# Kernel optimization log

Measured on AMD Instinct MI355X. Metric: run time of the kernel, lower is better.

Reference implementation:

```python
import math
import jax, jax.numpy as jnp
import numpy as np

B, S, E, H = 1, 2048, 2048, 16
HD = E // H // 2            # qk head dim = 64
DEPTH = 12
LAMBDA_INIT = 0.8 - 0.6 * math.exp(-0.3 * DEPTH)
EPS = 1e-5
NEG = -1e30

# rotary table (non-learned buffer), interleaved pairs, dim = HD
_pos = np.arange(S, dtype=np.float32)[:, None]
_div = np.exp(np.arange(0, HD, 2, dtype=np.float32) * (-math.log(10000.0) / HD))
COS = jnp.asarray(np.cos(_pos * _div))  # [S, HD/2]
SIN = jnp.asarray(np.sin(_pos * _div))


def _rope_interleaved(x):
    # x: [B, S, nH, HD]; rotate interleaved pairs (x0,x1),(x2,x3),...
    x1 = x[..., 0::2]
    x2 = x[..., 1::2]
    c = COS[None, :, None, :]
    s = SIN[None, :, None, :]
    o1 = x1 * c - x2 * s
    o2 = x1 * s + x2 * c
    return jnp.stack([o1, o2], axis=-1).reshape(x.shape)


def _causal_attn(q, k, v):
    # q,k: [B,S,H,Dk]; v: [B,S,H,Dv]; flash_attn default scale = Dk**-0.5
    scale = q.shape[-1] ** -0.5
    scores = jnp.einsum('bqhd,bkhd->bhqk', q, k) * scale
    mask = jnp.tril(jnp.ones((S, S), dtype=bool))
    scores = jnp.where(mask[None, None], scores, NEG)
    p = jax.nn.softmax(scores, axis=-1)
    return jnp.einsum('bhqk,bkhd->bqhd', p, v)


def setup_inputs() -> dict:
    key = jax.random.key(0)
    ks = jax.random.split(key, 10)
    w = lambda k: jax.random.normal(k, (E, E), dtype=jnp.float32) * 0.02
    lam = lambda k: jax.random.normal(k, (HD,), dtype=jnp.float32) * 0.1
    return {
        'x': jax.random.normal(ks[0], (B, S, E), dtype=jnp.float32),
        'Wq': w(ks[1]), 'Wk': w(ks[2]), 'Wv': w(ks[3]), 'Wo': w(ks[4]),
        'lq1': lam(ks[5]), 'lk1': lam(ks[6]), 'lq2': lam(ks[7]), 'lk2': lam(ks[8]),
        'g': jnp.ones((2 * HD,), dtype=jnp.float32),  # RMSNorm affine weight
    }


def reference(x, Wq, Wk, Wv, Wo, lq1, lk1, lq2, lk2, g):
    q = (x @ Wq).reshape(B, S, 2 * H, HD)
    k = (x @ Wk).reshape(B, S, 2 * H, HD)
    v = (x @ Wv).reshape(B, S, H, 2 * HD)
    q = _rope_interleaved(q).reshape(B, S, H, 2, HD)
    k = _rope_interleaved(k).reshape(B, S, H, 2, HD)
    q1, q2 = q[:, :, :, 0], q[:, :, :, 1]
    k1, k2 = k[:, :, :, 0], k[:, :, :, 1]
    attn1 = _causal_attn(q1, k1, v)  # [B,S,H,2*HD]
    attn2 = _causal_attn(q2, k2, v)
    lambda_full = (jnp.exp(jnp.sum(lq1 * lk1)) - jnp.exp(jnp.sum(lq2 * lk2))
                   + LAMBDA_INIT)
    a = attn1 - lambda_full * attn2
    # RMSNorm over last dim (2*HD) with affine weight g
    a = a * jax.lax.rsqrt(jnp.mean(a * a, axis=-1, keepdims=True) + EPS) * g
    a = a * (1.0 - LAMBDA_INIT)
    a = a.reshape(B, S, E)
    return a @ Wo
```

## Files before the change

kernel.cpp:

```cpp
#include <hip/hip_runtime.h>

typedef unsigned short u16;
typedef __bf16 bf16x8 __attribute__((ext_vector_type(8)));
typedef float f32x4 __attribute__((ext_vector_type(4)));

#define LAMBDA_INIT_F 0.7836057665f
#define ONE_MINUS_LI  0.2163942335f
#define Q_PRESCALE 0.1803368801f

__device__ __forceinline__ u16 f2bf(float f) {
  union { float f; unsigned u; } v; v.f = f;
  unsigned r = v.u + 0x7fffu + ((v.u >> 16) & 1u);
  return (u16)(r >> 16);
}

__device__ __forceinline__ float fast_exp2(float x) {
#if __has_builtin(__builtin_amdgcn_exp2f)
  return __builtin_amdgcn_exp2f(x);
#else
  return __builtin_exp2f(x);
#endif
}

__device__ __forceinline__ void gload_lds16(const void* g, void* l) {
  __builtin_amdgcn_global_load_lds(
      (const __attribute__((address_space(1))) void*)g,
      (__attribute__((address_space(3))) void*)l, 16, 0, 0);
}

__global__ __launch_bounds__(256) void cast_x_kernel(const float* __restrict__ x,
                                                     u16* __restrict__ xb) {
  const int i = (blockIdx.x * 256 + threadIdx.x) * 4;
  const float4 v = *(const float4*)(x + i);
  u16 tmp[4] = {f2bf(v.x), f2bf(v.y), f2bf(v.z), f2bf(v.w)};
  *(uint2*)(xb + i) = *(const uint2*)tmp;
}

__global__ __launch_bounds__(256) void transpose_w_kernel(
    const float* __restrict__ Wq, const float* __restrict__ Wk,
    const float* __restrict__ Wv, const float* __restrict__ Wo,
    u16* __restrict__ WqkvT, u16* __restrict__ WoT) {
  __shared__ float t[32][33];
  const int z = blockIdx.z;
  const float* src = (z == 0) ? Wq : (z == 1) ? Wk : (z == 2) ? Wv : Wo;
  const int n0 = blockIdx.x * 32, k0 = blockIdx.y * 32;
  const int tx = threadIdx.x & 31, ty = threadIdx.x >> 5;
#pragma unroll
  for (int i = 0; i < 4; ++i)
    t[ty + i * 8][tx] = src[(size_t)(k0 + ty + i * 8) * 2048 + n0 + tx];
  __syncthreads();
  u16* dst = (z < 3) ? (WqkvT + ((size_t)z * 2048 + n0) * 2048 + k0)
                     : (WoT + (size_t)n0 * 2048 + k0);
#pragma unroll
  for (int i = 0; i < 4; ++i)
    dst[(size_t)(ty + i * 8) * 2048 + tx] = f2bf(t[tx][ty + i * 8]);
}

__global__ __launch_bounds__(256) void rope_table_kernel(float* __restrict__ cosT,
                                                         float* __restrict__ sinT) {
  const int idx = blockIdx.x * 256 + threadIdx.x;
  const int s = idx >> 5, i = idx & 31;
  const float div = expf((float)(2 * i) * (-9.210340371976184f / 64.f));
  const float ang = (float)s * div;
  cosT[idx] = cosf(ang);
  sinT[idx] = sinf(ang);
}

__global__ void lambda_kernel(const float* __restrict__ lq1, const float* __restrict__ lk1,
                              const float* __restrict__ lq2, const float* __restrict__ lk2,
                              float* __restrict__ lam) {
  const int t = threadIdx.x;
  float p1 = lq1[t] * lk1[t];
  float p2 = lq2[t] * lk2[t];
#pragma unroll
  for (int mk = 1; mk < 64; mk <<= 1) {
    p1 += __shfl_xor(p1, mk);
    p2 += __shfl_xor(p2, mk);
  }
  if (t == 0) *lam = expf(p1) - expf(p2) + LAMBDA_INIT_F;
}

__global__ __launch_bounds__(256) void gemm_bt_kernel(
    const u16* __restrict__ A, const u16* __restrict__ Bt,
    float* __restrict__ C, int M, int N, int K) {
  __shared__ u16 As[2][128 * 64];
  __shared__ u16 Bs[2][128 * 64];
  const int tid = threadIdx.x;
  const int lane = tid & 63;
  const int w = tid >> 6;
  const int wm = w >> 1, wn = w & 1;
  const long m0 = (long)blockIdx.y * 128;
  const long n0 = (long)blockIdx.x * 128;

  f32x4 acc[4][4];
#pragma unroll
  for (int i = 0; i < 4; ++i)
#pragma unroll
    for (int j = 0; j < 4; ++j) acc[i][j] = f32x4{0.f, 0.f, 0.f, 0.f};

  const int sr = lane >> 3;
  const int scS = ((lane & 7) ^ sr) * 8;
  const int fr = lane & 15;
  const int kgrp = lane >> 4;
  const int swz = (fr & 7) << 3;

  const u16* aSrc = A + (m0 + w * 32 + sr) * (long)K + scS;
  const u16* bSrc = Bt + (n0 + w * 32 + sr) * (long)K + scS;

  auto stage = [&](int b, long koff) {
#pragma unroll
    for (int g = 0; g < 4; ++g) {
      gload_lds16(aSrc + koff + (size_t)g * 8 * K, &As[b][(w * 32 + g * 8) * 64]);
      gload_lds16(bSrc + koff + (size_t)g * 8 * K, &Bs[b][(w * 32 + g * 8) * 64]);
    }
  };

  stage(0, 0);
  __syncthreads();
  int cur = 0;
  for (int k0 = 0; k0 < K; k0 += 64) {
    if (k0 + 64 < K) stage(cur ^ 1, k0 + 64);
    __builtin_amdgcn_s_setprio(1);
#pragma unroll
    for (int ks = 0; ks < 2; ++ks) {
      bf16x8 af[4], bfr[4];
#pragma unroll
      for (int mi = 0; mi < 4; ++mi)
        af[mi] = *(const bf16x8*)&As[cur][(wm * 64 + mi * 16 + fr) * 64 +
                                          ((ks * 32 + kgrp * 8) ^ swz)];
#pragma unroll
      for (int ni = 0; ni < 4; ++ni)
        bfr[ni] = *(const bf16x8*)&Bs[cur][(wn * 64 + ni * 16 + fr) * 64 +
                                           ((ks * 32 + kgrp * 8) ^ swz)];
#pragma unroll
      for (int mi = 0; mi < 4; ++mi)
#pragma unroll
        for (int ni = 0; ni < 4; ++ni)
          acc[mi][ni] =
              __builtin_amdgcn_mfma_f32_16x16x32_bf16(af[mi], bfr[ni], acc[mi][ni], 0, 0, 0);
    }
    __builtin_amdgcn_s_setprio(0);
    __syncthreads();
    cur ^= 1;
  }
  const int rg = (lane >> 4) * 4;
#pragma unroll
  for (int mi = 0; mi < 4; ++mi)
#pragma unroll
    for (int ni = 0; ni < 4; ++ni) {
      const long col = n0 + wn * 64 + ni * 16 + fr;
#pragma unroll
      for (int j = 0; j < 4; ++j) {
        const long row = m0 + wm * 64 + mi * 16 + rg + j;
        C[row * N + col] = acc[mi][ni][j];
      }
    }
}

__global__ __launch_bounds__(256) void rope_apply_kernel(
    const float* __restrict__ proj, const float* __restrict__ cosT,
    const float* __restrict__ sinT, u16* __restrict__ Qh, u16* __restrict__ Kh) {
  const int s = blockIdx.x;
  const int tid = threadIdx.x;
#pragma unroll
  for (int t = 0; t < 8; ++t) {
    const int p = t * 256 + tid;
    const int isK = p >> 10;
    const int pp = p & 1023;
    const int hh = pp >> 5, i = pp & 31;
    const float* src = proj + (size_t)s * 6144 + isK * 2048 + hh * 64 + 2 * i;
    const float x1 = src[0], x2 = src[1];
    const float c = cosT[s * 32 + i], sn = sinT[s * 32 + i];
    const float scl = isK ? 1.0f : Q_PRESCALE;
    u16* dst = (isK ? Kh : Qh) + ((size_t)hh * 2048 + s) * 64 + 2 * i;
    dst[0] = f2bf((x1 * c - x2 * sn) * scl);
    dst[1] = f2bf((x1 * sn + x2 * c) * scl);
  }
}

__global__ __launch_bounds__(256) void transpose_v_kernel(const float* __restrict__ proj,
                                                          u16* __restrict__ Vt) {
  __shared__ float t[32][33];
  const int s0 = blockIdx.x * 32, r0 = blockIdx.y * 32;
  const int tx = threadIdx.x & 31, ty = threadIdx.x >> 5;
#pragma unroll
  for (int i = 0; i < 4; ++i)
    t[ty + i * 8][tx] = proj[(size_t)(s0 + ty + i * 8) * 6144 + 4096 + r0 + tx];
  __syncthreads();
#pragma unroll
  for (int i = 0; i < 4; ++i)
    Vt[(size_t)(r0 + ty + i * 8) * 2048 + s0 + tx] = f2bf(t[tx][ty + i * 8]);
}

__global__ __launch_bounds__(256) void attn_kernel(
    const u16* __restrict__ Qh, const u16* __restrict__ Kh,
    const u16* __restrict__ Vt, float* __restrict__ attnOut) {
  __shared__ u16 Kt[2][64 * 64];
  __shared__ u16 Vs[2][128 * 64];
  __shared__ __bf16 Ps[4 * 16 * 64];
  const int tid = threadIdx.x, lane = tid & 63, w = tid >> 6;
  const int fr = lane & 15, kgrp = lane >> 4;
  const int bid = blockIdx.x;
  const int xcd = bid & 7, idx = bid >> 3;
  const int hh = xcd * 4 + (idx & 3);
  const int pairIdx = idx >> 2;
  const int h = hh >> 1, comp = hh & 1;
  const int q0A = pairIdx * 64, q0B = (31 - pairIdx) * 64;
  const int jmaxA = pairIdx, jmaxB = 31 - pairIdx;
  const int ntA = jmaxA + 1, ntot = ntA + jmaxB + 1;

  const int sr = lane >> 3;
  const int scS = (((lane & 7) ^ sr) * 8);
  const int swz = (fr & 7) << 3;

  bf16x8 qf0, qf1;
  {
    const u16* qb = Qh + ((size_t)hh * 2048 + q0A + w * 16 + fr) * 64 + kgrp * 8;
    qf0 = *(const bf16x8*)qb;
    qf1 = *(const bf16x8*)(qb + 32);
  }
  bf16x8 onesf;
#pragma unroll
  for (int i = 0; i < 8; ++i) onesf[i] = (__bf16)1.0f;

  f32x4 o[9];
#pragma unroll
  for (int i = 0; i < 9; ++i) o[i] = f32x4{0.f, 0.f, 0.f, 0.f};
  float m_r[4] = {-1e30f, -1e30f, -1e30f, -1e30f};

  auto stage = [&](int b, int kv0) {
#pragma unroll
    for (int i = 0; i < 2; ++i)
      gload_lds16(Kh + ((size_t)hh * 2048 + kv0 + i * 32 + w * 8 + sr) * 64 + scS,
                  &Kt[b][(i * 32 + w * 8) * 64]);
#pragma unroll
    for (int i = 0; i < 4; ++i)
      gload_lds16(Vt + ((size_t)h * 128 + i * 32 + w * 8 + sr) * 2048 + kv0 + scS,
                  &Vs[b][(i * 32 + w * 8) * 64]);
  };

  auto writeOut = [&](int q0) {
    float* outp = attnOut + (size_t)comp * (2048 * 2048);
#pragma unroll
    for (int j = 0; j < 4; ++j) {
      const int row = q0 + w * 16 + kgrp * 4 + j;
      const float inv = 1.0f / o[8][j];
      float* op = outp + (size_t)row * 2048 + h * 128;
#pragma unroll
      for (int nf = 0; nf < 8; ++nf) op[nf * 16 + fr] = o[nf][j] * inv;
    }
  };

  stage(0, 0);
  __syncthreads();

  for (int t = 0; t < ntot; ++t) {
    const int cur = t & 1;
    if (t + 1 < ntot) {
      const int nk = (t + 1 < ntA) ? (t + 1) * 64 : (t + 1 - ntA) * 64;
      stage(cur ^ 1, nk);
    }
    const bool inA = t < ntA;
    const int q0 = inA ? q0A : q0B;
    const int jj = inA ? t : t - ntA;
    const int kv0 = jj * 64;
    const bool diag = inA ? (jj == jmaxA) : (jj == jmaxB);

    f32x4 s[4];
    __builtin_amdgcn_s_setprio(1);
#pragma unroll
    for (int nf = 0; nf < 4; ++nf) {
      s[nf] = f32x4{0.f, 0.f, 0.f, 0.f};
      const bf16x8 b0 = *(const bf16x8*)&Kt[cur][(nf * 16 + fr) * 64 + ((kgrp * 8) ^ swz)];
      const bf16x8 b1 =
          *(const bf16x8*)&Kt[cur][(nf * 16 + fr) * 64 + ((32 + kgrp * 8) ^ swz)];
      s[nf] = __builtin_amdgcn_mfma_f32_16x16x32_bf16(qf0, b0, s[nf], 0, 0, 0);
      s[nf] = __builtin_amdgcn_mfma_f32_16x16x32_bf16(qf1, b1, s[nf], 0, 0, 0);
    }
    __builtin_amdgcn_s_setprio(0);

    float pmax[4] = {-1e30f, -1e30f, -1e30f, -1e30f};
    if (diag) {
#pragma unroll
      for (int nf = 0; nf < 4; ++nf) {
        const int key = kv0 + nf * 16 + fr;
#pragma unroll
        for (int j = 0; j < 4; ++j) {
          float sc2 = s[nf][j];
          if (key > q0 + w * 16 + kgrp * 4 + j) sc2 = -1e30f;
          s[nf][j] = sc2;
          pmax[j] = fmaxf(pmax[j], sc2);
        }
      }
    } else {
#pragma unroll
      for (int nf = 0; nf < 4; ++nf)
#pragma unroll
        for (int j = 0; j < 4; ++j) pmax[j] = fmaxf(pmax[j], s[nf][j]);
    }
#pragma unroll
    for (int j = 0; j < 4; ++j)
#pragma unroll
      for (int mk = 1; mk < 16; mk <<= 1) pmax[j] = fmaxf(pmax[j], __shfl_xor(pmax[j], mk));

    bool grow = false;
#pragma unroll
    for (int j = 0; j < 4; ++j) grow |= (pmax[j] > m_r[j]);
    if (__any(grow)) {
#pragma unroll
      for (int j = 0; j < 4; ++j) {
        const float mn = fmaxf(m_r[j], pmax[j]);
        const float sf = fast_exp2(m_r[j] - mn);
        m_r[j] = mn;
#pragma unroll
        for (int nf = 0; nf < 9; ++nf) o[nf][j] *= sf;
      }
    }

#pragma unroll
    for (int nf = 0; nf < 4; ++nf)
#pragma unroll
      for (int j = 0; j < 4; ++j) {
        const float p = fast_exp2(s[nf][j] - m_r[j]);
        const int prow = kgrp * 4 + j;
        Ps[w * 1024 + prow * 64 + ((nf * 16 + fr) ^ ((prow & 7) << 3))] = (__bf16)p;
      }

    const bf16x8 pa0 = *(const bf16x8*)&Ps[w * 1024 + fr * 64 + ((kgrp * 8) ^ swz)];
    const bf16x8 pa1 = *(const bf16x8*)&Ps[w * 1024 + fr * 64 + ((32 + kgrp * 8) ^ swz)];
    __builtin_amdgcn_s_setprio(1);
#pragma unroll
    for (int nf = 0; nf < 8; ++nf) {
      const bf16x8 v0 = *(const bf16x8*)&Vs[cur][(nf * 16 + fr) * 64 + ((kgrp * 8) ^ swz)];
      const bf16x8 v1 =
          *(const bf16x8*)&Vs[cur][(nf * 16 + fr) * 64 + ((32 + kgrp * 8) ^ swz)];
      o[nf] = __builtin_amdgcn_mfma_f32_16x16x32_bf16(pa0, v0, o[nf], 0, 0, 0);
      o[nf] = __builtin_amdgcn_mfma_f32_16x16x32_bf16(pa1, v1, o[nf], 0, 0, 0);
    }
    o[8] = __builtin_amdgcn_mfma_f32_16x16x32_bf16(pa0, onesf, o[8], 0, 0, 0);
    o[8] = __builtin_amdgcn_mfma_f32_16x16x32_bf16(pa1, onesf, o[8], 0, 0, 0);
    __builtin_amdgcn_s_setprio(0);

    if (t == jmaxA) {
      writeOut(q0A);
#pragma unroll
      for (int i = 0; i < 9; ++i) o[i] = f32x4{0.f, 0.f, 0.f, 0.f};
#pragma unroll
      for (int j = 0; j < 4; ++j) m_r[j] = -1e30f;
      const u16* qb = Qh + ((size_t)hh * 2048 + q0B + w * 16 + fr) * 64 + kgrp * 8;
      qf0 = *(const bf16x8*)qb;
      qf1 = *(const bf16x8*)(qb + 32);
    }
    __syncthreads();
  }
  writeOut(q0B);
}

__global__ __launch_bounds__(256) void combine_kernel(
    const float* __restrict__ attn, const float* __restrict__ lam,
    const float* __restrict__ g, u16* __restrict__ ab) {
  const int lane = threadIdx.x & 63;
  const int idx = blockIdx.x * 4 + (threadIdx.x >> 6);
  const int s = idx >> 4, h = idx & 15;
  const float lf = *lam;
  const float* a1 = attn + (size_t)s * 2048 + h * 128;
  const float* a2 = a1 + (size_t)2048 * 2048;
  const float x0 = a1[lane] - lf * a2[lane];
  const float x1 = a1[lane + 64] - lf * a2[lane + 64];
  float ss = x0 * x0 + x1 * x1;
#pragma unroll
  for (int mk = 1; mk < 64; mk <<= 1) ss += __shfl_xor(ss, mk);
  const float r = rsqrtf(ss * (1.0f / 128.0f) + 1e-5f) * ONE_MINUS_LI;
  u16* op = ab + (size_t)s * 2048 + h * 128;
  op[lane] = f2bf(x0 * r * g[lane]);
  op[lane + 64] = f2bf(x1 * r * g[lane + 64]);
}

extern "C" void kernel_launch(void* const* d_in, const int* in_sizes, int n_in,
                              void* d_out, int out_size, void* d_ws, size_t ws_size,
                              hipStream_t stream) {
  const float* x = (const float*)d_in[0];
  const float* Wq = (const float*)d_in[1];
  const float* Wk = (const float*)d_in[2];
  const float* Wv = (const float*)d_in[3];
  const float* Wo = (const float*)d_in[4];
  const float* lq1 = (const float*)d_in[5];
  const float* lk1 = (const float*)d_in[6];
  const float* lq2 = (const float*)d_in[7];
  const float* lk2 = (const float*)d_in[8];
  const float* g = (const float*)d_in[9];
  float* out = (float*)d_out;

  char* ws = (char*)d_ws;
  u16* xb = (u16*)(ws);
  u16* WqkvT = (u16*)(ws + (size_t)(8u << 20));
  u16* WoT = (u16*)(ws + (size_t)(32u << 20));
  float* proj = (float*)(ws + (size_t)(40u << 20));
  float* attn = proj;
  u16* Qh = (u16*)(ws + (size_t)(88u << 20));
  u16* Kh = (u16*)(ws + (size_t)(96u << 20));
  u16* Vt = (u16*)(ws + (size_t)(104u << 20));
  u16* ab = (u16*)(ws + (size_t)(112u << 20));
  float* cosT = (float*)(ws + (size_t)(120u << 20));
  float* sinT = (float*)(ws + (size_t)(120u << 20) + (256u << 10));
  float* lam = (float*)(ws + (size_t)(120u << 20) + (512u << 10));

  cast_x_kernel<<<4096, 256, 0, stream>>>(x, xb);
  transpose_w_kernel<<<dim3(64, 64, 4), 256, 0, stream>>>(Wq, Wk, Wv, Wo, WqkvT, WoT);
  rope_table_kernel<<<256, 256, 0, stream>>>(cosT, sinT);
  lambda_kernel<<<1, 64, 0, stream>>>(lq1, lk1, lq2, lk2, lam);
  gemm_bt_kernel<<<dim3(48, 16), 256, 0, stream>>>(xb, WqkvT, proj, 2048, 6144, 2048);
  rope_apply_kernel<<<2048, 256, 0, stream>>>(proj, cosT, sinT, Qh, Kh);
  transpose_v_kernel<<<dim3(64, 64), 256, 0, stream>>>(proj, Vt);
  attn_kernel<<<512, 256, 0, stream>>>(Qh, Kh, Vt, attn);
  combine_kernel<<<8192, 256, 0, stream>>>(attn, lam, g, ab);
  gemm_bt_kernel<<<dim3(16, 16), 256, 0, stream>>>(ab, WoT, out, 2048, 2048, 2048);
}
```

Before: 338.8 us.

## Fuse prep kernels into one launch and fold RoPE/V-transpose into QKV GEMM epilogue

Merges the x cast, weight transposes, rope table and lambda computation into a single prep kernel so fewer kernels are launched. The QKV GEMM epilogue now applies RoPE and Q prescaling directly, writing bf16 Q/K per head and a transposed bf16 V. This removes the fp32 projection buffer round trip and two separate elementwise kernels. In exchange the epilogue does scattered 2-byte stores, column-strided for Vt, plus cos/sin table loads per element, which may be less coalesced than the old transpose kernels.

```diff
diff --git a/kernel.cpp b/kernel.cpp
--- a/kernel.cpp
+++ b/kernel.cpp
@@ -28,61 +28,63 @@
       (__attribute__((address_space(3))) void*)l, 16, 0, 0);
 }
 
-__global__ __launch_bounds__(256) void cast_x_kernel(const float* __restrict__ x,
-                                                     u16* __restrict__ xb) {
-  const int i = (blockIdx.x * 256 + threadIdx.x) * 4;
-  const float4 v = *(const float4*)(x + i);
-  u16 tmp[4] = {f2bf(v.x), f2bf(v.y), f2bf(v.z), f2bf(v.w)};
-  *(uint2*)(xb + i) = *(const uint2*)tmp;
-}
-
-__global__ __launch_bounds__(256) void transpose_w_kernel(
-    const float* __restrict__ Wq, const float* __restrict__ Wk,
-    const float* __restrict__ Wv, const float* __restrict__ Wo,
-    u16* __restrict__ WqkvT, u16* __restrict__ WoT) {
+__global__ __launch_bounds__(256) void prep_kernel(
+    const float* __restrict__ x, const float* __restrict__ Wq,
+    const float* __restrict__ Wk, const float* __restrict__ Wv,
+    const float* __restrict__ Wo, const float* __restrict__ lq1,
+    const float* __restrict__ lk1, const float* __restrict__ lq2,
+    const float* __restrict__ lk2, u16* __restrict__ xb,
+    u16* __restrict__ WqkvT, u16* __restrict__ WoT,
+    float* __restrict__ cosT, float* __restrict__ sinT, float* __restrict__ lam) {
   __shared__ float t[32][33];
-  const int z = blockIdx.z;
-  const float* src = (z == 0) ? Wq : (z == 1) ? Wk : (z == 2) ? Wv : Wo;
-  const int n0 = blockIdx.x * 32, k0 = blockIdx.y * 32;
-  const int tx = threadIdx.x & 31, ty = threadIdx.x >> 5;
-#pragma unroll
-  for (int i = 0; i < 4; ++i)
-    t[ty + i * 8][tx] = src[(size_t)(k0 + ty + i * 8) * 2048 + n0 + tx];
-  __syncthreads();
-  u16* dst = (z < 3) ? (WqkvT + ((size_t)z * 2048 + n0) * 2048 + k0)
-                     : (WoT + (size_t)n0 * 2048 + k0);
-#pragma unroll
-  for (int i = 0; i < 4; ++i)
-    dst[(size_t)(ty + i * 8) * 2048 + tx] = f2bf(t[tx][ty + i * 8]);
-}
-
-__global__ __launch_bounds__(256) void rope_table_kernel(float* __restrict__ cosT,
-                                                         float* __restrict__ sinT) {
-  const int idx = blockIdx.x * 256 + threadIdx.x;
-  const int s = idx >> 5, i = idx & 31;
-  const float div = expf((float)(2 * i) * (-9.210340371976184f / 64.f));
-  const float ang = (float)s * div;
-  cosT[idx] = cosf(ang);
-  sinT[idx] = sinf(ang);
-}
-
-__global__ void lambda_kernel(const float* __restrict__ lq1, const float* __restrict__ lk1,
-                              const float* __restrict__ lq2, const float* __restrict__ lk2,
-                              float* __restrict__ lam) {
-  const int t = threadIdx.x;
-  float p1 = lq1[t] * lk1[t];
-  float p2 = lq2[t] * lk2[t];
-#pragma unroll
-  for (int mk = 1; mk < 64; mk <<= 1) {
-    p1 += __shfl_xor(p1, mk);
-    p2 += __shfl_xor(p2, mk);
+  const int bid = blockIdx.x;
+  const int tid = threadIdx.x;
+  if (bid < 16384) {
+    const int z = bid >> 12;
+    const int rem = bid & 4095;
+    const int n0 = (rem & 63) * 32, k0 = (rem >> 6) * 32;
+    const float* src = (z == 0) ? Wq : (z == 1) ? Wk : (z == 2) ? Wv : Wo;
+    const int tx = tid & 31, ty = tid >> 5;
+#pragma unroll
+    for (int i = 0; i < 4; ++i)
+      t[ty + i * 8][tx] = src[(size_t)(k0 + ty + i * 8) * 2048 + n0 + tx];
+    __syncthreads();
+    u16* dst = (z < 3) ? (WqkvT + ((size_t)z * 2048 + n0) * 2048 + k0)
+                       : (WoT + (size_t)n0 * 2048 + k0);
+#pragma unroll
+    for (int i = 0; i < 4; ++i)
+      dst[(size_t)(ty + i * 8) * 2048 + tx] = f2bf(t[tx][ty + i * 8]);
+  } else if (bid < 16384 + 4096) {
+    const int i = ((bid - 16384) * 256 + tid) * 4;
+    const float4 v = *(const float4*)(x + i);
+    u16 tmp[4] = {f2bf(v.x), f2bf(v.y), f2bf(v.z), f2bf(v.w)};
+    *(uint2*)(xb + i) = *(const uint2*)tmp;
+  } else if (bid < 16384 + 4096 + 256) {
+    const int idx = (bid - 16384 - 4096) * 256 + tid;
+    const int s = idx >> 5, i = idx & 31;
+    const float div = expf((float)(2 * i) * (-9.210340371976184f / 64.f));
+    const float ang = (float)s * div;
+    cosT[idx] = cosf(ang);
+    sinT[idx] = sinf(ang);
+  } else {
+    if (tid < 64) {
+      float p1 = lq1[tid] * lk1[tid];
+      float p2 = lq2[tid] * lk2[tid];
+#pragma unroll
+      for (int mk = 1; mk < 64; mk <<= 1) {
+        p1 += __shfl_xor(p1, mk);
+        p2 += __shfl_xor(p2, mk);
+      }
+      if (tid == 0) *lam = expf(p1) - expf(p2) + LAMBDA_INIT_F;
+    }
   }
-  if (t == 0) *lam = expf(p1) - expf(p2) + LAMBDA_INIT_F;
 }
 
 __global__ __launch_bounds__(256) void gemm_bt_kernel(
     const u16* __restrict__ A, const u16* __restrict__ Bt,
-    float* __restrict__ C, int M, int N, int K) {
+    float* __restrict__ C, int M, int N, int K, int mode,
+    const float* __restrict__ cosT, const float* __restrict__ sinT,
+    u16* __restrict__ Qh, u16* __restrict__ Kh, u16* __restrict__ Vt) {
   __shared__ u16 As[2][128 * 64];
   __shared__ u16 Bs[2][128 * 64];
   const int tid = threadIdx.x;
@@ -144,52 +146,52 @@
     cur ^= 1;
   }
   const int rg = (lane >> 4) * 4;
-#pragma unroll
-  for (int mi = 0; mi < 4; ++mi)
-#pragma unroll
-    for (int ni = 0; ni < 4; ++ni) {
-      const long col = n0 + wn * 64 + ni * 16 + fr;
-#pragma unroll
-      for (int j = 0; j < 4; ++j) {
-        const long row = m0 + wm * 64 + mi * 16 + rg + j;
-        C[row * N + col] = acc[mi][ni][j];
-      }
-    }
-}
-
-__global__ __launch_bounds__(256) void rope_apply_kernel(
-    const float* __restrict__ proj, const float* __restrict__ cosT,
-    const float* __restrict__ sinT, u16* __restrict__ Qh, u16* __restrict__ Kh) {
-  const int s = blockIdx.x;
-  const int tid = threadIdx.x;
-#pragma unroll
-  for (int t = 0; t < 8; ++t) {
-    const int p = t * 256 + tid;
-    const int isK = p >> 10;
-    const int pp = p & 1023;
-    const int hh = pp >> 5, i = pp & 31;
-    const float* src = proj + (size_t)s * 6144 + isK * 2048 + hh * 64 + 2 * i;
-    const float x1 = src[0], x2 = src[1];
-    const float c = cosT[s * 32 + i], sn = sinT[s * 32 + i];
+  if (mode == 0) {
+#pragma unroll
+    for (int mi = 0; mi < 4; ++mi)
+#pragma unroll
+      for (int ni = 0; ni < 4; ++ni) {
+        const long col = n0 + wn * 64 + ni * 16 + fr;
+#pragma unroll
+        for (int j = 0; j < 4; ++j) {
+          const long row = m0 + wm * 64 + mi * 16 + rg + j;
+          C[row * N + col] = acc[mi][ni][j];
+        }
+      }
+  } else if (n0 >= 4096) {
+#pragma unroll
+    for (int mi = 0; mi < 4; ++mi)
+#pragma unroll
+      for (int ni = 0; ni < 4; ++ni) {
+        const long vr = n0 - 4096 + wn * 64 + ni * 16 + fr;
+#pragma unroll
+        for (int j = 0; j < 4; ++j) {
+          const long row = m0 + wm * 64 + mi * 16 + rg + j;
+          Vt[vr * 2048 + row] = f2bf(acc[mi][ni][j]);
+        }
+      }
+  } else {
+    const int isK = (int)(n0 >> 11);
+    u16* dstBase = isK ? Kh : Qh;
     const float scl = isK ? 1.0f : Q_PRESCALE;
-    u16* dst = (isK ? Kh : Qh) + ((size_t)hh * 2048 + s) * 64 + 2 * i;
-    dst[0] = f2bf((x1 * c - x2 * sn) * scl);
-    dst[1] = f2bf((x1 * sn + x2 * c) * scl);
+#pragma unroll
+    for (int mi = 0; mi < 4; ++mi)
+#pragma unroll
+      for (int ni = 0; ni < 4; ++ni) {
+        const int col = (int)(n0 & 2047) + wn * 64 + ni * 16 + fr;
+        const int hh = col >> 6, d = col & 63, i2 = (col & 63) >> 1;
+        const bool odd = d & 1;
+#pragma unroll
+        for (int j = 0; j < 4; ++j) {
+          const int row = (int)m0 + wm * 64 + mi * 16 + rg + j;
+          const float v = acc[mi][ni][j];
+          const float p = __shfl_xor(v, 1);
+          const float c = cosT[row * 32 + i2], sn = sinT[row * 32 + i2];
+          const float outv = odd ? (p * sn + v * c) : (v * c - p * sn);
+          dstBase[((size_t)hh * 2048 + row) * 64 + d] = f2bf(outv * scl);
+        }
+      }
   }
-}
-
-__global__ __launch_bounds__(256) void transpose_v_kernel(const float* __restrict__ proj,
-                                                          u16* __restrict__ Vt) {
-  __shared__ float t[32][33];
-  const int s0 = blockIdx.x * 32, r0 = blockIdx.y * 32;
-  const int tx = threadIdx.x & 31, ty = threadIdx.x >> 5;
-#pragma unroll
-  for (int i = 0; i < 4; ++i)
-    t[ty + i * 8][tx] = proj[(size_t)(s0 + ty + i * 8) * 6144 + 4096 + r0 + tx];
-  __syncthreads();
-#pragma unroll
-  for (int i = 0; i < 4; ++i)
-    Vt[(size_t)(r0 + ty + i * 8) * 2048 + s0 + tx] = f2bf(t[tx][ty + i * 8]);
 }
 
 __global__ __launch_bounds__(256) void attn_kernel(
@@ -395,8 +397,7 @@
   u16* xb = (u16*)(ws);
   u16* WqkvT = (u16*)(ws + (size_t)(8u << 20));
   u16* WoT = (u16*)(ws + (size_t)(32u << 20));
-  float* proj = (float*)(ws + (size_t)(40u << 20));
-  float* attn = proj;
+  float* attn = (float*)(ws + (size_t)(40u << 20));
   u16* Qh = (u16*)(ws + (size_t)(88u << 20));
   u16* Kh = (u16*)(ws + (size_t)(96u << 20));
   u16* Vt = (u16*)(ws + (size_t)(104u << 20));
@@ -405,14 +406,13 @@
   float* sinT = (float*)(ws + (size_t)(120u << 20) + (256u << 10));
   float* lam = (float*)(ws + (size_t)(120u << 20) + (512u << 10));
 
-  cast_x_kernel<<<4096, 256, 0, stream>>>(x, xb);
-  transpose_w_kernel<<<dim3(64, 64, 4), 256, 0, stream>>>(Wq, Wk, Wv, Wo, WqkvT, WoT);
-  rope_table_kernel<<<256, 256, 0, stream>>>(cosT, sinT);
-  lambda_kernel<<<1, 64, 0, stream>>>(lq1, lk1, lq2, lk2, lam);
-  gemm_bt_kernel<<<dim3(48, 16), 256, 0, stream>>>(xb, WqkvT, proj, 2048, 6144, 2048);
-  rope_apply_kernel<<<2048, 256, 0, stream>>>(proj, cosT, sinT, Qh, Kh);
-  transpose_v_kernel<<<dim3(64, 64), 256, 0, stream>>>(proj, Vt);
+  prep_kernel<<<16384 + 4096 + 256 + 1, 256, 0, stream>>>(
+      x, Wq, Wk, Wv, Wo, lq1, lk1, lq2, lk2, xb, WqkvT, WoT, cosT, sinT, lam);
+  gemm_bt_kernel<<<dim3(48, 16), 256, 0, stream>>>(xb, WqkvT, nullptr, 2048, 6144, 2048,
+                                                   1, cosT, sinT, Qh, Kh, Vt);
   attn_kernel<<<512, 256, 0, stream>>>(Qh, Kh, Vt, attn);
   combine_kernel<<<8192, 256, 0, stream>>>(attn, lam, g, ab);
-  gemm_bt_kernel<<<dim3(16, 16), 256, 0, stream>>>(ab, WoT, out, 2048, 2048, 2048);
-}
+  gemm_bt_kernel<<<dim3(16, 16), 256, 0, stream>>>(ab, WoT, out, 2048, 2048, 2048,
+                                                   0, nullptr, nullptr, nullptr, nullptr,
+                                                   nullptr);
+}
```

After: 316.0 us. 1.07x faster.
